# Kernel optimization log

Measured on AMD Instinct MI355X. Metric: run time of the kernel, lower is better.

Reference implementation:

```python
import jax, jax.numpy as jnp
import numpy as np

NB_T, NB_C = 4, 4
B, LT, LC, D, H = 32, 256, 128, 256, 8
E = D // H
SCALE = 1.0 / float(np.sqrt(E))


def full_attention(x, Wq, bq, Wk, bk, Wv, bv, Wo, bo):
    # x: [B, L, D]; multi-head full attention (no mask, eval-mode dropout)
    Bx, L, Dx = x.shape
    q = (x @ Wq + bq).reshape(Bx, L, H, E)
    k = (x @ Wk + bk).reshape(Bx, L, H, E)
    v = (x @ Wv + bv).reshape(Bx, L, H, E)
    scores = jnp.einsum('blhe,bshe->bhls', q, k)
    A = jax.nn.softmax(scores * SCALE, axis=-1)
    out = jnp.einsum('bhls,bshd->blhd', A, v).reshape(Bx, L, Dx)
    return out @ Wo + bo


def _branch(x, Wq, bq, Wk, bk, Wv, bv, Wo, bo, Wqi, bqi, Wki, bki, Wvi, bvi, Woi, boi):
    # x: [nb, B, L, D]; per-block intra attention (distinct weights per block)
    x_intra = jax.vmap(full_attention)(x, Wq, bq, Wk, bk, Wv, bv, Wo, bo)
    # router tokens = last token of each block -> [B, nb, D]
    routers = jnp.transpose(x_intra[:, :, -1, :], (1, 0, 2))
    x_inter = full_attention(routers, Wqi, bqi, Wki, bki, Wvi, bvi, Woi, boi)
    x_inter = jnp.transpose(x_inter, (1, 0, 2))[:, :, None, :]  # [nb, B, 1, D]
    # replace each block's router token with its inter-attended version
    return jnp.concatenate([x_intra[:, :, :-1, :], x_inter], axis=2)


def setup_inputs():
    key = jax.random.key(0)
    ks = jax.random.split(key, 32)
    s = 0.02
    inp = {}
    inp['x_t'] = jax.random.normal(ks[0], (NB_T, B, LT, D), jnp.float32)
    inp['x_c'] = jax.random.normal(ks[1], (NB_C, B, LC, D), jnp.float32)
    i = 2
    for pfx, nb in (('t', NB_T), ('c', NB_C)):
        for nm in ('q', 'k', 'v', 'o'):
            inp['W%s_%s' % (nm, pfx)] = jax.random.normal(ks[i], (nb, D, D), jnp.float32) * s
            i += 1
            inp['b%s_%s' % (nm, pfx)] = jnp.zeros((nb, D), jnp.float32)
    for pfx in ('it', 'ic'):
        for nm in ('q', 'k', 'v', 'o'):
            inp['W%s_%s' % (nm, pfx)] = jax.random.normal(ks[i], (D, D), jnp.float32) * s
            i += 1
            inp['b%s_%s' % (nm, pfx)] = jnp.zeros((D,), jnp.float32)
    return inp


def reference(x_t, x_c, Wq_t, bq_t, Wk_t, bk_t, Wv_t, bv_t, Wo_t, bo_t, Wq_c, bq_c, Wk_c, bk_c, Wv_c, bv_c, Wo_c, bo_c, Wq_it, bq_it, Wk_it, bk_it, Wv_it, bv_it, Wo_it, bo_it, Wq_ic, bq_ic, Wk_ic, bk_ic, Wv_ic, bv_ic, Wo_ic, bo_ic):
    x_out_t = _branch(x_t, Wq_t, bq_t, Wk_t, bk_t, Wv_t, bv_t, Wo_t, bo_t,
                      Wq_it, bq_it, Wk_it, bk_it, Wv_it, bv_it, Wo_it, bo_it)
    x_out_c = _branch(x_c, Wq_c, bq_c, Wk_c, bk_c, Wv_c, bv_c, Wo_c, bo_c,
                      Wq_ic, bq_ic, Wk_ic, bk_ic, Wv_ic, bv_ic, Wo_ic, bo_ic)
    return (x_out_t, x_out_c)
```

## Files before the change

kernel.cpp:

```cpp
#include <hip/hip_runtime.h>
#include <hip/hip_bf16.h>
#include <stdint.h>

#define DMODEL 256
#define HEADS 8
#define EHEAD 32
#define BATCH 32
#define NB 4
#define LT 256
#define LC 128
#define SCALE_F 0.17677669529663687f

typedef __attribute__((ext_vector_type(8))) short short8;
typedef __attribute__((ext_vector_type(4))) float f32x4;
typedef __attribute__((ext_vector_type(4))) unsigned short us4;

#define ASG __attribute__((address_space(1)))
#define ASL __attribute__((address_space(3)))

__device__ __forceinline__ unsigned short bf16_rn(float f) {
    unsigned u = __float_as_uint(f);
    u += 0x7FFFu + ((u >> 16) & 1u);
    return (unsigned short)(u >> 16);
}
__device__ __forceinline__ float bf16_f(unsigned short h) {
    return __uint_as_float(((unsigned)h) << 16);
}

__global__ void split_hi_lo(const float* __restrict__ src, unsigned short* __restrict__ hi,
                            unsigned short* __restrict__ lo, int n4)
{
    int i = blockIdx.x * blockDim.x + threadIdx.x;
    int stride = gridDim.x * blockDim.x;
    for (; i < n4; i += stride) {
        float4 a = ((const float4*)src)[i];
        float v[4] = {a.x, a.y, a.z, a.w};
        us4 h, l;
        #pragma unroll
        for (int j = 0; j < 4; ++j) {
            unsigned short hh = bf16_rn(v[j]);
            h[j] = hh;
            l[j] = bf16_rn(v[j] - bf16_f(hh));
        }
        ((us4*)hi)[i] = h;
        ((us4*)lo)[i] = l;
    }
}

__global__ __launch_bounds__(256) void transpose_split(
    const float* __restrict__ W0, const float* __restrict__ W1,
    const float* __restrict__ W2, const float* __restrict__ W3,
    unsigned short* __restrict__ H0, unsigned short* __restrict__ L0,
    unsigned short* __restrict__ H1, unsigned short* __restrict__ L1,
    unsigned short* __restrict__ H2, unsigned short* __restrict__ L2,
    unsigned short* __restrict__ H3, unsigned short* __restrict__ L3,
    int per_set)
{
    const int z   = blockIdx.z;
    const int set = z / per_set;
    const int zi  = z - set * per_set;
    const float* W; unsigned short *H, *L;
    if      (set == 0) { W = W0; H = H0; L = L0; }
    else if (set == 1) { W = W1; H = H1; L = L1; }
    else if (set == 2) { W = W2; H = H2; L = L2; }
    else               { W = W3; H = H3; L = L3; }
    W += (long long)zi * 65536;
    H += (long long)zi * 65536;
    L += (long long)zi * 65536;

    __shared__ float tile[64][65];
    const int k0 = blockIdx.y * 64, n0 = blockIdx.x * 64;
    const int c = threadIdx.x & 63, r4 = threadIdx.x >> 6;

    #pragma unroll
    for (int i = 0; i < 16; ++i) {
        int kl = r4 + i * 4;
        tile[kl][c] = W[(long long)(k0 + kl) * 256 + n0 + c];
    }
    __syncthreads();
    #pragma unroll
    for (int i = 0; i < 16; ++i) {
        int nl = r4 + i * 4;
        float v = tile[c][nl];
        unsigned short hh = bf16_rn(v);
        unsigned short ll = bf16_rn(v - bf16_f(hh));
        long long o = (long long)(n0 + nl) * 256 + k0 + c;
        H[o] = hh;
        L[o] = ll;
    }
}

template<int OUT_MODE>
__global__ __launch_bounds__(256, 2) void gemm_bf16x3_t(
    const unsigned short* __restrict__ Ah, const unsigned short* __restrict__ Al,
    const unsigned short* __restrict__ Bh, const unsigned short* __restrict__ Bl,
    const float* __restrict__ bias, void* __restrict__ Cv, float scale,
    long long sA, long long sW, long long sBias, long long sC)
{
    const int z = blockIdx.z;
    const char* aH = (const char*)(Ah + z * sA);
    const char* aL = (const char*)(Al + z * sA);
    const char* bH = (const char*)(Bh + z * sW);
    const char* bL = (const char*)(Bl + z * sW);
    const float* bz = bias + z * sBias;

    const int bm = blockIdx.y * 128;
    const int bn = blockIdx.x * 128;
    const int tid = threadIdx.x;
    const int w = tid >> 6, l = tid & 63;
    const int wr = w >> 1, wc = w & 1;
    const int lr = l & 15, lk = l >> 4;

    __shared__ __align__(16) unsigned short lds[16384];
    unsigned short* lAh = lds;
    unsigned short* lAl = lds + 4096;
    unsigned short* lBh = lds + 8192;
    unsigned short* lBl = lds + 12288;

    const int g0 = w * 64 + l;
    const int g1 = g0 + 256;
    const int row0 = g0 >> 2, kq0 = (g0 & 3) ^ ((row0 >> 1) & 3);
    const int row1 = g1 >> 2, kq1 = (g1 & 3) ^ ((row1 >> 1) & 3);
    const long long offA0 = (long long)(bm + row0) * 512 + kq0 * 16;
    const long long offA1 = (long long)(bm + row1) * 512 + kq1 * 16;
    const long long offB0 = (long long)(bn + row0) * 512 + kq0 * 16;
    const long long offB1 = (long long)(bn + row1) * 512 + kq1 * 16;

    f32x4 acc[4][4];
    #pragma unroll
    for (int m = 0; m < 4; ++m)
        #pragma unroll
        for (int n = 0; n < 4; ++n)
            acc[m][n] = (f32x4){0.f, 0.f, 0.f, 0.f};

    for (int k0 = 0; k0 < 256; k0 += 32) {
        const long long kb = (long long)k0 * 2;
        __builtin_amdgcn_global_load_lds((const ASG unsigned int*)(aH + offA0 + kb),
                                         (ASL unsigned int*)&lAh[g0 * 8], 16, 0, 0);
        __builtin_amdgcn_global_load_lds((const ASG unsigned int*)(aH + offA1 + kb),
                                         (ASL unsigned int*)&lAh[g1 * 8], 16, 0, 0);
        __builtin_amdgcn_global_load_lds((const ASG unsigned int*)(aL + offA0 + kb),
                                         (ASL unsigned int*)&lAl[g0 * 8], 16, 0, 0);
        __builtin_amdgcn_global_load_lds((const ASG unsigned int*)(aL + offA1 + kb),
                                         (ASL unsigned int*)&lAl[g1 * 8], 16, 0, 0);
        __builtin_amdgcn_global_load_lds((const ASG unsigned int*)(bH + offB0 + kb),
                                         (ASL unsigned int*)&lBh[g0 * 8], 16, 0, 0);
        __builtin_amdgcn_global_load_lds((const ASG unsigned int*)(bH + offB1 + kb),
                                         (ASL unsigned int*)&lBh[g1 * 8], 16, 0, 0);
        __builtin_amdgcn_global_load_lds((const ASG unsigned int*)(bL + offB0 + kb),
                                         (ASL unsigned int*)&lBl[g0 * 8], 16, 0, 0);
        __builtin_amdgcn_global_load_lds((const ASG unsigned int*)(bL + offB1 + kb),
                                         (ASL unsigned int*)&lBl[g1 * 8], 16, 0, 0);
        asm volatile("s_waitcnt vmcnt(0)" ::: "memory");
        __syncthreads();

        short8 fah[4], fal[4], fbh[4], fbl[4];
        #pragma unroll
        for (int m = 0; m < 4; ++m) {
            int row = wr * 64 + m * 16 + lr;
            int off = row * 32 + ((lk ^ ((row >> 1) & 3)) * 8);
            fah[m] = *(const short8*)&lAh[off];
            fal[m] = *(const short8*)&lAl[off];
        }
        #pragma unroll
        for (int n = 0; n < 4; ++n) {
            int row = wc * 64 + n * 16 + lr;
            int off = row * 32 + ((lk ^ ((row >> 1) & 3)) * 8);
            fbh[n] = *(const short8*)&lBh[off];
            fbl[n] = *(const short8*)&lBl[off];
        }
        #pragma unroll
        for (int m = 0; m < 4; ++m)
            #pragma unroll
            for (int n = 0; n < 4; ++n) {
                acc[m][n] = __builtin_amdgcn_mfma_f32_16x16x32_bf16(fah[m], fbh[n], acc[m][n], 0, 0, 0);
                acc[m][n] = __builtin_amdgcn_mfma_f32_16x16x32_bf16(fal[m], fbh[n], acc[m][n], 0, 0, 0);
                acc[m][n] = __builtin_amdgcn_mfma_f32_16x16x32_bf16(fah[m], fbl[n], acc[m][n], 0, 0, 0);
            }
        __syncthreads();
    }

    #pragma unroll
    for (int n = 0; n < 4; ++n) {
        const int col = bn + wc * 64 + n * 16 + lr;
        const float bv = bz[col];
        #pragma unroll
        for (int m = 0; m < 4; ++m) {
            const int row = bm + wr * 64 + m * 16 + lk * 4;
            #pragma unroll
            for (int j = 0; j < 4; ++j) {
                float v = acc[m][n][j] + bv;
                if (OUT_MODE == 0) {
                    ((float*)Cv)[z * sC + (long long)(row + j) * 256 + col] = v;
                } else {
                    ((unsigned short*)Cv)[z * sC + (long long)(row + j) * 256 + col] =
                        bf16_rn(v * scale);
                }
            }
        }
    }
}

template<int L>
__global__ __launch_bounds__(256) void v_transpose(
    const unsigned short* __restrict__ Vbf, unsigned short* __restrict__ VT)
{
    __shared__ unsigned short tile[L * 36];
    const int h = blockIdx.x, blkb = blockIdx.y, tid = threadIdx.x;
    const unsigned short* src = Vbf + (long long)blkb * L * 256 + h * 32;
    unsigned short* dst = VT + ((long long)blkb * HEADS + h) * 32 * L;

    #pragma unroll
    for (int i = 0; i < L * 8 / 256; ++i) {
        int ci = i * 256 + tid;
        int kv = ci >> 3, e0 = (ci & 7) * 4;
        us4 v = *(const us4*)(src + (long long)kv * 256 + e0);
        *(us4*)(&tile[kv * 36 + e0]) = v;
    }
    __syncthreads();
    #pragma unroll
    for (int i = 0; i < L * 8 / 256; ++i) {
        int ci = i * 256 + tid;
        int e = ci / (L / 4), kvc = ci % (L / 4);
        us4 v;
        #pragma unroll
        for (int j = 0; j < 4; ++j) v[j] = tile[(kvc * 4 + j) * 36 + e];
        *(us4*)(dst + (long long)e * L + kvc * 4) = v;
    }
}

template<int L>
__global__ __launch_bounds__(256) void attn_mfma(
    const unsigned short* __restrict__ Qbf, const unsigned short* __restrict__ Kbf,
    const unsigned short* __restrict__ VT,
    unsigned short* __restrict__ AOh, unsigned short* __restrict__ AOl)
{
    constexpr int KV_FRAGS    = L / 16;
    constexpr int PV_STEPS    = L / 32;
    constexpr int QT_PER_WAVE = L / 64;
    constexpr int K_BYTES     = L * 64;
    constexpr int GPR         = L / 8;

    __shared__ __align__(16) char smem[L * 256];
    unsigned short* Ks  = (unsigned short*)smem;
    unsigned short* VTs = (unsigned short*)(smem + K_BYTES);
    unsigned short* Pa  = (unsigned short*)(smem + 2 * K_BYTES);

    const int h    = blockIdx.x;
    const int blkb = blockIdx.y;
    const int tid  = threadIdx.x;
    const int w    = tid >> 6;
    const int l    = tid & 63;
    const int lq   = l & 15;
    const int lg   = l >> 4;

    const long long rowbase = (long long)blkb * L;
    const unsigned short* Kh = Kbf + rowbase * 256 + h * 32;
    const unsigned short* Qh = Qbf + rowbase * 256 + h * 32;
    const unsigned short* Vh = VT + ((long long)blkb * HEADS + h) * (32 * L);

    #pragma unroll
    for (int i = 0; i < K_BYTES / 16 / 256; ++i) {
        int gi = i * 256 + tid;
        int row = gi >> 2;
        int gsrc = (gi & 3) ^ ((row >> 1) & 3);
        __builtin_amdgcn_global_load_lds(
            (const ASG unsigned int*)(Kh + (long long)row * 256 + gsrc * 8),
            (ASL unsigned int*)(Ks + gi * 8), 16, 0, 0);
    }
    #pragma unroll
    for (int i = 0; i < K_BYTES / 16 / 256; ++i) {
        int gi = i * 256 + tid;
        int e  = gi / GPR;
        int gsrc = (gi % GPR) ^ (e & 7);
        __builtin_amdgcn_global_load_lds(
            (const ASG unsigned int*)(Vh + (long long)e * L + gsrc * 8),
            (ASL unsigned int*)(VTs + gi * 8), 16, 0, 0);
    }
    asm volatile("s_waitcnt vmcnt(0)" ::: "memory");
    __syncthreads();

    unsigned short* Pw = Pa + w * (16 * L);

    for (int qt = 0; qt < QT_PER_WAVE; ++qt) {
        const int q0 = w * (QT_PER_WAVE * 16) + qt * 16;
        short8 qf = *(const short8*)(Qh + (long long)(q0 + lq) * 256 + lg * 8);

        f32x4 sf[KV_FRAGS];
        #pragma unroll
        for (int t = 0; t < KV_FRAGS; ++t) {
            int row = t * 16 + lq;
            int off = row * 32 + ((lg ^ ((row >> 1) & 3)) * 8);
            short8 kf = *(const short8*)(Ks + off);
            sf[t] = __builtin_amdgcn_mfma_f32_16x16x32_bf16(kf, qf,
                        (f32x4){0.f, 0.f, 0.f, 0.f}, 0, 0, 0);
        }
        float lsum = 0.f;
        unsigned short pb[KV_FRAGS][4];
        #pragma unroll
        for (int t = 0; t < KV_FRAGS; ++t)
            #pragma unroll
            for (int j = 0; j < 4; ++j) {
                float s = fminf(fmaxf(sf[t][j], -60.f), 60.f);
                float p = __builtin_exp2f(s);
                lsum += p;
                pb[t][j] = bf16_rn(p);
            }
        lsum += __shfl_xor(lsum, 16);
        lsum += __shfl_xor(lsum, 32);

        #pragma unroll
        for (int t = 0; t < KV_FRAGS; ++t) {
            us4 v; v[0] = pb[t][0]; v[1] = pb[t][1]; v[2] = pb[t][2]; v[3] = pb[t][3];
            int slot = (t * 4 + lg) ^ (lq & 14);
            *(us4*)(Pw + lq * L + slot * 4) = v;
        }
        asm volatile("s_waitcnt lgkmcnt(0)" ::: "memory");

        f32x4 oacc[2] = {(f32x4){0.f,0.f,0.f,0.f}, (f32x4){0.f,0.f,0.f,0.f}};
        #pragma unroll
        for (int s = 0; s < PV_STEPS; ++s) {
            int pslot = (s * 8 + lg * 2) ^ (lq & 14);
            short8 pf = *(const short8*)(Pw + lq * L + pslot * 4);
            #pragma unroll
            for (int et = 0; et < 2; ++et) {
                int e = et * 16 + lq;
                int gk = (s * 4 + lg) ^ (e & 7);
                short8 vf = *(const short8*)(VTs + e * L + gk * 8);
                oacc[et] = __builtin_amdgcn_mfma_f32_16x16x32_bf16(pf, vf, oacc[et], 0, 0, 0);
            }
        }
        float inv[4];
        #pragma unroll
        for (int j = 0; j < 4; ++j)
            inv[j] = 1.f / __shfl(lsum, lg * 4 + j);
        #pragma unroll
        for (int et = 0; et < 2; ++et)
            #pragma unroll
            for (int j = 0; j < 4; ++j) {
                long long row = rowbase + q0 + lg * 4 + j;
                int col = h * 32 + et * 16 + lq;
                float o = oacc[et][j] * inv[j];
                unsigned short hi = bf16_rn(o);
                unsigned short lo = bf16_rn(o - bf16_f(hi));
                AOh[row * 256 + col] = hi;
                AOl[row * 256 + col] = lo;
            }
    }
}

__global__ void gather_routers(const float* __restrict__ xi, float* __restrict__ rt, int L)
{
    int t = blockIdx.x * blockDim.x + threadIdx.x;
    int d = t & 255;
    int r = t >> 8;
    int i = r & 3;
    int b = r >> 2;
    rt[(long long)r * DMODEL + d] =
        xi[(((long long)i * BATCH + b) * L + (L - 1)) * DMODEL + d];
}

__global__ void inter_attn(const float* __restrict__ RQ, const float* __restrict__ RK,
                           const float* __restrict__ RV, float* __restrict__ RA)
{
    int t = blockIdx.x * blockDim.x + threadIdx.x;
    int l = t & 3;
    int h = (t >> 2) & 7;
    int b = t >> 5;

    float q[EHEAD];
    #pragma unroll
    for (int e = 0; e < EHEAD; ++e)
        q[e] = RQ[((long long)b * 4 + l) * DMODEL + h * EHEAD + e];

    float sc[4];
    float m = -1e30f;
    #pragma unroll
    for (int s = 0; s < 4; ++s) {
        float d = 0.f;
        #pragma unroll
        for (int e = 0; e < EHEAD; ++e)
            d = fmaf(q[e], RK[((long long)b * 4 + s) * DMODEL + h * EHEAD + e], d);
        sc[s] = d * SCALE_F;
        m = fmaxf(m, sc[s]);
    }
    float lsum = 0.f;
    #pragma unroll
    for (int s = 0; s < 4; ++s) { sc[s] = __expf(sc[s] - m); lsum += sc[s]; }
    const float inv = 1.f / lsum;

    #pragma unroll
    for (int e = 0; e < EHEAD; ++e) {
        float a = 0.f;
        #pragma unroll
        for (int s = 0; s < 4; ++s)
            a = fmaf(sc[s], RV[((long long)b * 4 + s) * DMODEL + h * EHEAD + e], a);
        RA[((long long)b * 4 + l) * DMODEL + h * EHEAD + e] = a * inv;
    }
}

__global__ void scatter_routers(const float* __restrict__ ro, float* __restrict__ xi, int L)
{
    int t = blockIdx.x * blockDim.x + threadIdx.x;
    int d = t & 255;
    int r = t >> 8;
    int i = r & 3;
    int b = r >> 2;
    xi[(((long long)i * BATCH + b) * L + (L - 1)) * DMODEL + d] =
        ro[(long long)r * DMODEL + d];
}

struct BranchScratch {
    unsigned short *xh, *xl;
    unsigned short *Qbf, *Kbf, *Vbf, *VTb, *AOh, *AOl;
    unsigned short *Wth[4], *Wtl[4];
    unsigned short *WtIh[4], *WtIl[4];
    float *RT, *RQ, *RK, *RV, *RA, *RO;
    unsigned short *RTh, *RTl, *RAh, *RAl;
};

template<int L>
static void run_branch(const float* x,
    const float* Wq, const float* bq, const float* Wk, const float* bk,
    const float* Wv, const float* bv, const float* Wo, const float* bo,
    const float* Wqi, const float* bqi, const float* Wki, const float* bki,
    const float* Wvi, const float* bvi, const float* Woi, const float* boi,
    float* out, const BranchScratch& S, hipStream_t stream)
{
    const int M = BATCH * L;
    const long long sX = (long long)M * DMODEL;
    const int nTot = NB * M * DMODEL;
    const float CS = 0.17677669529663687f * 1.4426950408889634f;

    split_hi_lo<<<1024, 256, 0, stream>>>(x, S.xh, S.xl, nTot / 4);
    transpose_split<<<dim3(4, 4, 16), 256, 0, stream>>>(
        Wq, Wk, Wv, Wo,
        S.Wth[0], S.Wtl[0], S.Wth[1], S.Wtl[1],
        S.Wth[2], S.Wtl[2], S.Wth[3], S.Wtl[3], 4);

    dim3 gProj(2, M / 128, NB);
    gemm_bf16x3_t<1><<<gProj, 256, 0, stream>>>(S.xh, S.xl, S.Wth[0], S.Wtl[0], bq, S.Qbf, CS,   sX, 65536, 256, sX);
    gemm_bf16x3_t<1><<<gProj, 256, 0, stream>>>(S.xh, S.xl, S.Wth[1], S.Wtl[1], bk, S.Kbf, 1.0f, sX, 65536, 256, sX);
    gemm_bf16x3_t<1><<<gProj, 256, 0, stream>>>(S.xh, S.xl, S.Wth[2], S.Wtl[2], bv, S.Vbf, 1.0f, sX, 65536, 256, sX);

    v_transpose<L><<<dim3(HEADS, NB * BATCH), 256, 0, stream>>>(S.Vbf, S.VTb);
    attn_mfma<L><<<dim3(HEADS, NB * BATCH), 256, 0, stream>>>(S.Qbf, S.Kbf, S.VTb, S.AOh, S.AOl);

    gemm_bf16x3_t<0><<<gProj, 256, 0, stream>>>(S.AOh, S.AOl, S.Wth[3], S.Wtl[3], bo, out, 1.0f, sX, 65536, 256, sX);

    gather_routers<<<128, 256, 0, stream>>>(out, S.RT, L);
    split_hi_lo<<<32, 256, 0, stream>>>(S.RT, S.RTh, S.RTl, 128 * DMODEL / 4);
    transpose_split<<<dim3(4, 4, 4), 256, 0, stream>>>(
        Wqi, Wki, Wvi, Woi,
        S.WtIh[0], S.WtIl[0], S.WtIh[1], S.WtIl[1],
        S.WtIh[2], S.WtIl[2], S.WtIh[3], S.WtIl[3], 1);

    dim3 gI(2, 1, 1);
    gemm_bf16x3_t<0><<<gI, 256, 0, stream>>>(S.RTh, S.RTl, S.WtIh[0], S.WtIl[0], bqi, S.RQ, 1.0f, 0, 0, 0, 0);
    gemm_bf16x3_t<0><<<gI, 256, 0, stream>>>(S.RTh, S.RTl, S.WtIh[1], S.WtIl[1], bki, S.RK, 1.0f, 0, 0, 0, 0);
    gemm_bf16x3_t<0><<<gI, 256, 0, stream>>>(S.RTh, S.RTl, S.WtIh[2], S.WtIl[2], bvi, S.RV, 1.0f, 0, 0, 0, 0);

    inter_attn<<<4, 256, 0, stream>>>(S.RQ, S.RK, S.RV, S.RA);

    split_hi_lo<<<32, 256, 0, stream>>>(S.RA, S.RAh, S.RAl, 128 * DMODEL / 4);
    gemm_bf16x3_t<0><<<gI, 256, 0, stream>>>(S.RAh, S.RAl, S.WtIh[3], S.WtIl[3], boi, S.RO, 1.0f, 0, 0, 0, 0);

    scatter_routers<<<128, 256, 0, stream>>>(S.RO, out, L);
}

extern "C" void kernel_launch(void* const* d_in, const int* in_sizes, int n_in,
                              void* d_out, int out_size, void* d_ws, size_t ws_size,
                              hipStream_t stream)
{
    const float* x_t  = (const float*)d_in[0];
    const float* x_c  = (const float*)d_in[1];
    const float* Wq_t = (const float*)d_in[2];  const float* bq_t = (const float*)d_in[3];
    const float* Wk_t = (const float*)d_in[4];  const float* bk_t = (const float*)d_in[5];
    const float* Wv_t = (const float*)d_in[6];  const float* bv_t = (const float*)d_in[7];
    const float* Wo_t = (const float*)d_in[8];  const float* bo_t = (const float*)d_in[9];
    const float* Wq_c = (const float*)d_in[10]; const float* bq_c = (const float*)d_in[11];
    const float* Wk_c = (const float*)d_in[12]; const float* bk_c = (const float*)d_in[13];
    const float* Wv_c = (const float*)d_in[14]; const float* bv_c = (const float*)d_in[15];
    const float* Wo_c = (const float*)d_in[16]; const float* bo_c = (const float*)d_in[17];
    const float* Wq_it = (const float*)d_in[18]; const float* bq_it = (const float*)d_in[19];
    const float* Wk_it = (const float*)d_in[20]; const float* bk_it = (const float*)d_in[21];
    const float* Wv_it = (const float*)d_in[22]; const float* bv_it = (const float*)d_in[23];
    const float* Wo_it = (const float*)d_in[24]; const float* bo_it = (const float*)d_in[25];
    const float* Wq_ic = (const float*)d_in[26]; const float* bq_ic = (const float*)d_in[27];
    const float* Wk_ic = (const float*)d_in[28]; const float* bk_ic = (const float*)d_in[29];
    const float* Wv_ic = (const float*)d_in[30]; const float* bv_ic = (const float*)d_in[31];
    const float* Wo_ic = (const float*)d_in[32]; const float* bo_ic = (const float*)d_in[33];

    float* out = (float*)d_out;

    char* p = (char*)d_ws;
    auto alloc = [&](size_t bytes) -> char* {
        char* r = p;
        p += (bytes + 255) & ~(size_t)255;
        return r;
    };
    const size_t QKV = (size_t)NB * BATCH * LT * DMODEL;

    BranchScratch S;
    S.xh  = (unsigned short*)alloc(QKV * 2);
    S.xl  = (unsigned short*)alloc(QKV * 2);
    S.Qbf = (unsigned short*)alloc(QKV * 2);
    S.Kbf = (unsigned short*)alloc(QKV * 2);
    S.Vbf = (unsigned short*)alloc(QKV * 2);
    S.VTb = (unsigned short*)alloc(QKV * 2);
    S.AOh = (unsigned short*)alloc(QKV * 2);
    S.AOl = (unsigned short*)alloc(QKV * 2);
    for (int i = 0; i < 4; ++i) {
        S.Wth[i] = (unsigned short*)alloc((size_t)NB * 65536 * 2);
        S.Wtl[i] = (unsigned short*)alloc((size_t)NB * 65536 * 2);
    }
    for (int i = 0; i < 4; ++i) {
        S.WtIh[i] = (unsigned short*)alloc(65536 * 2);
        S.WtIl[i] = (unsigned short*)alloc(65536 * 2);
    }
    S.RT = (float*)alloc(128 * DMODEL * 4);
    S.RQ = (float*)alloc(128 * DMODEL * 4);
    S.RK = (float*)alloc(128 * DMODEL * 4);
    S.RV = (float*)alloc(128 * DMODEL * 4);
    S.RA = (float*)alloc(128 * DMODEL * 4);
    S.RO = (float*)alloc(128 * DMODEL * 4);
    S.RTh = (unsigned short*)alloc(128 * DMODEL * 2);
    S.RTl = (unsigned short*)alloc(128 * DMODEL * 2);
    S.RAh = (unsigned short*)alloc(128 * DMODEL * 2);
    S.RAl = (unsigned short*)alloc(128 * DMODEL * 2);

    run_branch<LT>(x_t, Wq_t, bq_t, Wk_t, bk_t, Wv_t, bv_t, Wo_t, bo_t,
                   Wq_it, bq_it, Wk_it, bk_it, Wv_it, bv_it, Wo_it, bo_it,
                   out, S, stream);

    float* out_c = out + (size_t)NB * BATCH * LT * DMODEL;
    run_branch<LC>(x_c, Wq_c, bq_c, Wk_c, bk_c, Wv_c, bv_c, Wo_c, bo_c,
                   Wq_ic, bq_ic, Wk_ic, bk_ic, Wv_ic, bv_ic, Wo_ic, bo_ic,
                   out_c, S, stream);
}
```

Measured before the change: 516.0 us.

## Fuse QKV projections with V-transpose epilogue and merge small prep/split kernels

Combines the three Q/K/V projection GEMMs into one launch whose V epilogue writes the head-transposed layout directly, removing the separate V buffer and transpose kernel. Weight prep for intra and inter weights is merged into a single launch, and hi/lo bf16 splitting is folded into the router gather and inter-attention kernels. The inter-attention QKV GEMMs are batched into one launch, and the attention kernel's P staging is reorganized per step. Scattered 2-byte stores for V^T and a higher occupancy target may cost bandwidth or registers.

```diff
diff --git a/kernel.cpp b/kernel.cpp
--- a/kernel.cpp
+++ b/kernel.cpp
@@ -9,7 +9,6 @@
 #define NB 4
 #define LT 256
 #define LC 128
-#define SCALE_F 0.17677669529663687f
 
 typedef __attribute__((ext_vector_type(8))) short short8;
 typedef __attribute__((ext_vector_type(4))) float f32x4;
@@ -47,26 +46,20 @@
     }
 }
 
-__global__ __launch_bounds__(256) void transpose_split(
-    const float* __restrict__ W0, const float* __restrict__ W1,
-    const float* __restrict__ W2, const float* __restrict__ W3,
-    unsigned short* __restrict__ H0, unsigned short* __restrict__ L0,
-    unsigned short* __restrict__ H1, unsigned short* __restrict__ L1,
-    unsigned short* __restrict__ H2, unsigned short* __restrict__ L2,
-    unsigned short* __restrict__ H3, unsigned short* __restrict__ L3,
-    int per_set)
-{
-    const int z   = blockIdx.z;
-    const int set = z / per_set;
-    const int zi  = z - set * per_set;
-    const float* W; unsigned short *H, *L;
-    if      (set == 0) { W = W0; H = H0; L = L0; }
-    else if (set == 1) { W = W1; H = H1; L = L1; }
-    else if (set == 2) { W = W2; H = H2; L = L2; }
-    else               { W = W3; H = H3; L = L3; }
-    W += (long long)zi * 65536;
-    H += (long long)zi * 65536;
-    L += (long long)zi * 65536;
+struct PrepArgs {
+    const float* W[8];
+    unsigned short* H[8];
+    unsigned short* Lo[8];
+};
+
+__global__ __launch_bounds__(256) void prep_weights(PrepArgs pa)
+{
+    const int z = blockIdx.z;
+    int set, zi;
+    if (z < 16) { set = z >> 2; zi = z & 3; } else { set = 4 + (z - 16); zi = 0; }
+    const float* W = pa.W[set] + (long long)zi * 65536;
+    unsigned short* H = pa.H[set] + (long long)zi * 65536;
+    unsigned short* L = pa.Lo[set] + (long long)zi * 65536;
 
     __shared__ float tile[64][65];
     const int k0 = blockIdx.y * 64, n0 = blockIdx.x * 64;
@@ -90,158 +83,180 @@
     }
 }
 
-template<int OUT_MODE>
-__global__ __launch_bounds__(256, 2) void gemm_bf16x3_t(
+#define GEMM_BODY(aH, aL, bH, bL)                                                   \
+    const int bm = blockIdx.y * 128;                                                \
+    const int bn = blockIdx.x * 128;                                                \
+    const int tid = threadIdx.x;                                                    \
+    const int w = tid >> 6, l = tid & 63;                                           \
+    const int wr = w >> 1, wc = w & 1;                                              \
+    const int lr = l & 15, lk = l >> 4;                                             \
+    __shared__ __align__(16) unsigned short lds[16384];                             \
+    unsigned short* lAh = lds;                                                      \
+    unsigned short* lAl = lds + 4096;                                               \
+    unsigned short* lBh = lds + 8192;                                               \
+    unsigned short* lBl = lds + 12288;                                              \
+    const int g0 = w * 64 + l;                                                      \
+    const int g1 = g0 + 256;                                                        \
+    const int row0 = g0 >> 2, kq0 = (g0 & 3) ^ ((row0 >> 1) & 3);                   \
+    const int row1 = g1 >> 2, kq1 = (g1 & 3) ^ ((row1 >> 1) & 3);                   \
+    const long long offA0 = (long long)(bm + row0) * 512 + kq0 * 16;                \
+    const long long offA1 = (long long)(bm + row1) * 512 + kq1 * 16;                \
+    const long long offB0 = (long long)(bn + row0) * 512 + kq0 * 16;                \
+    const long long offB1 = (long long)(bn + row1) * 512 + kq1 * 16;                \
+    f32x4 acc[4][4];                                                                \
+    _Pragma("unroll")                                                               \
+    for (int m = 0; m < 4; ++m)                                                     \
+        _Pragma("unroll")                                                           \
+        for (int n = 0; n < 4; ++n)                                                 \
+            acc[m][n] = (f32x4){0.f, 0.f, 0.f, 0.f};                                \
+    for (int k0 = 0; k0 < 256; k0 += 32) {                                          \
+        const long long kb = (long long)k0 * 2;                                     \
+        __builtin_amdgcn_global_load_lds((const ASG unsigned int*)(aH + offA0 + kb),\
+                                         (ASL unsigned int*)&lAh[g0 * 8], 16, 0, 0);\
+        __builtin_amdgcn_global_load_lds((const ASG unsigned int*)(aH + offA1 + kb),\
+                                         (ASL unsigned int*)&lAh[g1 * 8], 16, 0, 0);\
+        __builtin_amdgcn_global_load_lds((const ASG unsigned int*)(aL + offA0 + kb),\
+                                         (ASL unsigned int*)&lAl[g0 * 8], 16, 0, 0);\
+        __builtin_amdgcn_global_load_lds((const ASG unsigned int*)(aL + offA1 + kb),\
+                                         (ASL unsigned int*)&lAl[g1 * 8], 16, 0, 0);\
+        __builtin_amdgcn_global_load_lds((const ASG unsigned int*)(bH + offB0 + kb),\
+                                         (ASL unsigned int*)&lBh[g0 * 8], 16, 0, 0);\
+        __builtin_amdgcn_global_load_lds((const ASG unsigned int*)(bH + offB1 + kb),\
+                                         (ASL unsigned int*)&lBh[g1 * 8], 16, 0, 0);\
+        __builtin_amdgcn_global_load_lds((const ASG unsigned int*)(bL + offB0 + kb),\
+                                         (ASL unsigned int*)&lBl[g0 * 8], 16, 0, 0);\
+        __builtin_amdgcn_global_load_lds((const ASG unsigned int*)(bL + offB1 + kb),\
+                                         (ASL unsigned int*)&lBl[g1 * 8], 16, 0, 0);\
+        asm volatile("s_waitcnt vmcnt(0)" ::: "memory");                            \
+        __syncthreads();                                                            \
+        short8 fah[4], fal[4], fbh[4], fbl[4];                                      \
+        _Pragma("unroll")                                                           \
+        for (int m = 0; m < 4; ++m) {                                               \
+            int row = wr * 64 + m * 16 + lr;                                        \
+            int off = row * 32 + ((lk ^ ((row >> 1) & 3)) * 8);                     \
+            fah[m] = *(const short8*)&lAh[off];                                     \
+            fal[m] = *(const short8*)&lAl[off];                                     \
+        }                                                                           \
+        _Pragma("unroll")                                                           \
+        for (int n = 0; n < 4; ++n) {                                               \
+            int row = wc * 64 + n * 16 + lr;                                        \
+            int off = row * 32 + ((lk ^ ((row >> 1) & 3)) * 8);                     \
+            fbh[n] = *(const short8*)&lBh[off];                                     \
+            fbl[n] = *(const short8*)&lBl[off];                                     \
+        }                                                                           \
+        _Pragma("unroll")                                                           \
+        for (int m = 0; m < 4; ++m)                                                 \
+            _Pragma("unroll")                                                       \
+            for (int n = 0; n < 4; ++n) {                                           \
+                acc[m][n] = __builtin_amdgcn_mfma_f32_16x16x32_bf16(fah[m], fbh[n], acc[m][n], 0, 0, 0); \
+                acc[m][n] = __builtin_amdgcn_mfma_f32_16x16x32_bf16(fal[m], fbh[n], acc[m][n], 0, 0, 0); \
+                acc[m][n] = __builtin_amdgcn_mfma_f32_16x16x32_bf16(fah[m], fbl[n], acc[m][n], 0, 0, 0); \
+            }                                                                       \
+        __syncthreads();                                                            \
+    }
+
+__global__ __launch_bounds__(256, 3) void gemm_qkv(
     const unsigned short* __restrict__ Ah, const unsigned short* __restrict__ Al,
-    const unsigned short* __restrict__ Bh, const unsigned short* __restrict__ Bl,
-    const float* __restrict__ bias, void* __restrict__ Cv, float scale,
-    long long sA, long long sW, long long sBias, long long sC)
+    const unsigned short* __restrict__ Wbase,
+    const float* __restrict__ bq, const float* __restrict__ bk, const float* __restrict__ bv,
+    unsigned short* __restrict__ Qout, unsigned short* __restrict__ Kout,
+    unsigned short* __restrict__ VTout,
+    float qscale, int M, int kvShift)
+{
+    const int zAll = blockIdx.z;
+    const int proj = zAll >> 2;
+    const int zb   = zAll & 3;
+    const long long sX = (long long)M * 256;
+    const char* aH = (const char*)(Ah + zb * sX);
+    const char* aL = (const char*)(Al + zb * sX);
+    const long long wOff = (long long)proj * (2LL * NB * 65536) + (long long)zb * 65536;
+    const char* bH = (const char*)(Wbase + wOff);
+    const char* bL = (const char*)(Wbase + wOff + NB * 65536);
+    const float* bz = (proj == 0 ? bq : proj == 1 ? bk : bv) + zb * 256;
+
+    GEMM_BODY(aH, aL, bH, bL)
+
+    if (proj < 2) {
+        unsigned short* C = (proj == 0 ? Qout : Kout) + zb * sX;
+        const float sc = (proj == 0) ? qscale : 1.0f;
+        #pragma unroll
+        for (int n = 0; n < 4; ++n) {
+            const int col = bn + wc * 64 + n * 16 + lr;
+            const float bv_ = bz[col];
+            #pragma unroll
+            for (int m = 0; m < 4; ++m) {
+                const int row = bm + wr * 64 + m * 16 + lk * 4;
+                #pragma unroll
+                for (int j = 0; j < 4; ++j)
+                    C[(long long)(row + j) * 256 + col] = bf16_rn((acc[m][n][j] + bv_) * sc);
+            }
+        }
+    } else {
+        const int Lkv = 1 << kvShift;
+        #pragma unroll
+        for (int n = 0; n < 4; ++n) {
+            const int col = bn + wc * 64 + n * 16 + lr;
+            const int hh = col >> 5, e = col & 31;
+            const float bv_ = bz[col];
+            #pragma unroll
+            for (int m = 0; m < 4; ++m) {
+                const int row = bm + wr * 64 + m * 16 + lk * 4;
+                #pragma unroll
+                for (int j = 0; j < 4; ++j) {
+                    const int r = row + j;
+                    const int blkb = zb * BATCH + (r >> kvShift);
+                    const long long dst =
+                        ((((long long)blkb * HEADS + hh) * 32 + e) << kvShift) + (r & (Lkv - 1));
+                    VTout[dst] = bf16_rn(acc[m][n][j] + bv_);
+                }
+            }
+        }
+    }
+}
+
+struct Bias4 { const float* p[4]; };
+
+__global__ __launch_bounds__(256, 3) void gemm_f32out(
+    const unsigned short* __restrict__ Ah, const unsigned short* __restrict__ Al,
+    const unsigned short* __restrict__ Bh_, const unsigned short* __restrict__ Bl_,
+    Bias4 b4, float* __restrict__ C,
+    long long sA, long long sW, long long sC)
 {
     const int z = blockIdx.z;
     const char* aH = (const char*)(Ah + z * sA);
     const char* aL = (const char*)(Al + z * sA);
-    const char* bH = (const char*)(Bh + z * sW);
-    const char* bL = (const char*)(Bl + z * sW);
-    const float* bz = bias + z * sBias;
-
-    const int bm = blockIdx.y * 128;
-    const int bn = blockIdx.x * 128;
-    const int tid = threadIdx.x;
-    const int w = tid >> 6, l = tid & 63;
-    const int wr = w >> 1, wc = w & 1;
-    const int lr = l & 15, lk = l >> 4;
-
-    __shared__ __align__(16) unsigned short lds[16384];
-    unsigned short* lAh = lds;
-    unsigned short* lAl = lds + 4096;
-    unsigned short* lBh = lds + 8192;
-    unsigned short* lBl = lds + 12288;
-
-    const int g0 = w * 64 + l;
-    const int g1 = g0 + 256;
-    const int row0 = g0 >> 2, kq0 = (g0 & 3) ^ ((row0 >> 1) & 3);
-    const int row1 = g1 >> 2, kq1 = (g1 & 3) ^ ((row1 >> 1) & 3);
-    const long long offA0 = (long long)(bm + row0) * 512 + kq0 * 16;
-    const long long offA1 = (long long)(bm + row1) * 512 + kq1 * 16;
-    const long long offB0 = (long long)(bn + row0) * 512 + kq0 * 16;
-    const long long offB1 = (long long)(bn + row1) * 512 + kq1 * 16;
-
-    f32x4 acc[4][4];
-    #pragma unroll
-    for (int m = 0; m < 4; ++m)
-        #pragma unroll
-        for (int n = 0; n < 4; ++n)
-            acc[m][n] = (f32x4){0.f, 0.f, 0.f, 0.f};
-
-    for (int k0 = 0; k0 < 256; k0 += 32) {
-        const long long kb = (long long)k0 * 2;
-        __builtin_amdgcn_global_load_lds((const ASG unsigned int*)(aH + offA0 + kb),
-                                         (ASL unsigned int*)&lAh[g0 * 8], 16, 0, 0);
-        __builtin_amdgcn_global_load_lds((const ASG unsigned int*)(aH + offA1 + kb),
-                                         (ASL unsigned int*)&lAh[g1 * 8], 16, 0, 0);
-        __builtin_amdgcn_global_load_lds((const ASG unsigned int*)(aL + offA0 + kb),
-                                         (ASL unsigned int*)&lAl[g0 * 8], 16, 0, 0);
-        __builtin_amdgcn_global_load_lds((const ASG unsigned int*)(aL + offA1 + kb),
-                                         (ASL unsigned int*)&lAl[g1 * 8], 16, 0, 0);
-        __builtin_amdgcn_global_load_lds((const ASG unsigned int*)(bH + offB0 + kb),
-                                         (ASL unsigned int*)&lBh[g0 * 8], 16, 0, 0);
-        __builtin_amdgcn_global_load_lds((const ASG unsigned int*)(bH + offB1 + kb),
-                                         (ASL unsigned int*)&lBh[g1 * 8], 16, 0, 0);
-        __builtin_amdgcn_global_load_lds((const ASG unsigned int*)(bL + offB0 + kb),
-                                         (ASL unsigned int*)&lBl[g0 * 8], 16, 0, 0);
-        __builtin_amdgcn_global_load_lds((const ASG unsigned int*)(bL + offB1 + kb),
-                                         (ASL unsigned int*)&lBl[g1 * 8], 16, 0, 0);
-        asm volatile("s_waitcnt vmcnt(0)" ::: "memory");
-        __syncthreads();
-
-        short8 fah[4], fal[4], fbh[4], fbl[4];
-        #pragma unroll
-        for (int m = 0; m < 4; ++m) {
-            int row = wr * 64 + m * 16 + lr;
-            int off = row * 32 + ((lk ^ ((row >> 1) & 3)) * 8);
-            fah[m] = *(const short8*)&lAh[off];
-            fal[m] = *(const short8*)&lAl[off];
-        }
-        #pragma unroll
-        for (int n = 0; n < 4; ++n) {
-            int row = wc * 64 + n * 16 + lr;
-            int off = row * 32 + ((lk ^ ((row >> 1) & 3)) * 8);
-            fbh[n] = *(const short8*)&lBh[off];
-            fbl[n] = *(const short8*)&lBl[off];
-        }
-        #pragma unroll
-        for (int m = 0; m < 4; ++m)
-            #pragma unroll
-            for (int n = 0; n < 4; ++n) {
-                acc[m][n] = __builtin_amdgcn_mfma_f32_16x16x32_bf16(fah[m], fbh[n], acc[m][n], 0, 0, 0);
-                acc[m][n] = __builtin_amdgcn_mfma_f32_16x16x32_bf16(fal[m], fbh[n], acc[m][n], 0, 0, 0);
-                acc[m][n] = __builtin_amdgcn_mfma_f32_16x16x32_bf16(fah[m], fbl[n], acc[m][n], 0, 0, 0);
-            }
-        __syncthreads();
-    }
+    const char* bH = (const char*)(Bh_ + z * sW);
+    const char* bL = (const char*)(Bl_ + z * sW);
+    const float* bz = b4.p[z];
+
+    GEMM_BODY(aH, aL, bH, bL)
 
     #pragma unroll
     for (int n = 0; n < 4; ++n) {
         const int col = bn + wc * 64 + n * 16 + lr;
-        const float bv = bz[col];
+        const float bv_ = bz[col];
         #pragma unroll
         for (int m = 0; m < 4; ++m) {
             const int row = bm + wr * 64 + m * 16 + lk * 4;
             #pragma unroll
-            for (int j = 0; j < 4; ++j) {
-                float v = acc[m][n][j] + bv;
-                if (OUT_MODE == 0) {
-                    ((float*)Cv)[z * sC + (long long)(row + j) * 256 + col] = v;
-                } else {
-                    ((unsigned short*)Cv)[z * sC + (long long)(row + j) * 256 + col] =
-                        bf16_rn(v * scale);
-                }
-            }
+            for (int j = 0; j < 4; ++j)
+                C[z * sC + (long long)(row + j) * 256 + col] = acc[m][n][j] + bv_;
         }
     }
 }
 
 template<int L>
-__global__ __launch_bounds__(256) void v_transpose(
-    const unsigned short* __restrict__ Vbf, unsigned short* __restrict__ VT)
-{
-    __shared__ unsigned short tile[L * 36];
-    const int h = blockIdx.x, blkb = blockIdx.y, tid = threadIdx.x;
-    const unsigned short* src = Vbf + (long long)blkb * L * 256 + h * 32;
-    unsigned short* dst = VT + ((long long)blkb * HEADS + h) * 32 * L;
-
-    #pragma unroll
-    for (int i = 0; i < L * 8 / 256; ++i) {
-        int ci = i * 256 + tid;
-        int kv = ci >> 3, e0 = (ci & 7) * 4;
-        us4 v = *(const us4*)(src + (long long)kv * 256 + e0);
-        *(us4*)(&tile[kv * 36 + e0]) = v;
-    }
-    __syncthreads();
-    #pragma unroll
-    for (int i = 0; i < L * 8 / 256; ++i) {
-        int ci = i * 256 + tid;
-        int e = ci / (L / 4), kvc = ci % (L / 4);
-        us4 v;
-        #pragma unroll
-        for (int j = 0; j < 4; ++j) v[j] = tile[(kvc * 4 + j) * 36 + e];
-        *(us4*)(dst + (long long)e * L + kvc * 4) = v;
-    }
-}
-
-template<int L>
-__global__ __launch_bounds__(256) void attn_mfma(
+__global__ __launch_bounds__(256, 4) void attn_mfma(
     const unsigned short* __restrict__ Qbf, const unsigned short* __restrict__ Kbf,
     const unsigned short* __restrict__ VT,
     unsigned short* __restrict__ AOh, unsigned short* __restrict__ AOl)
 {
-    constexpr int KV_FRAGS    = L / 16;
-    constexpr int PV_STEPS    = L / 32;
     constexpr int QT_PER_WAVE = L / 64;
-    constexpr int K_BYTES     = L * 64;
-    constexpr int GPR         = L / 8;
-
-    __shared__ __align__(16) char smem[L * 256];
+    constexpr int NS      = L / 32;
+    constexpr int K_BYTES = L * 64;
+    constexpr int GPR     = L / 8;
+
+    __shared__ __align__(16) char smem[2 * K_BYTES + 4 * 2048];
     unsigned short* Ks  = (unsigned short*)smem;
     unsigned short* VTs = (unsigned short*)(smem + K_BYTES);
     unsigned short* Pa  = (unsigned short*)(smem + 2 * K_BYTES);
@@ -253,11 +268,19 @@
     const int l    = tid & 63;
     const int lq   = l & 15;
     const int lg   = l >> 4;
+    const int a3   = (lq >> 2) & 3;
 
     const long long rowbase = (long long)blkb * L;
     const unsigned short* Kh = Kbf + rowbase * 256 + h * 32;
     const unsigned short* Qh = Qbf + rowbase * 256 + h * 32;
     const unsigned short* Vh = VT + ((long long)blkb * HEADS + h) * (32 * L);
+
+    short8 qf[QT_PER_WAVE];
+    #pragma unroll
+    for (int qt = 0; qt < QT_PER_WAVE; ++qt) {
+        int q0 = w * (QT_PER_WAVE * 16) + qt * 16;
+        qf[qt] = *(const short8*)(Qh + (long long)(q0 + lq) * 256 + lg * 8);
+    }
 
     #pragma unroll
     for (int i = 0; i < K_BYTES / 16 / 256; ++i) {
@@ -280,48 +303,39 @@
     asm volatile("s_waitcnt vmcnt(0)" ::: "memory");
     __syncthreads();
 
-    unsigned short* Pw = Pa + w * (16 * L);
-
+    unsigned short* Pw = Pa + w * 1024;
+
+    #pragma unroll
     for (int qt = 0; qt < QT_PER_WAVE; ++qt) {
         const int q0 = w * (QT_PER_WAVE * 16) + qt * 16;
-        short8 qf = *(const short8*)(Qh + (long long)(q0 + lq) * 256 + lg * 8);
-
-        f32x4 sf[KV_FRAGS];
-        #pragma unroll
-        for (int t = 0; t < KV_FRAGS; ++t) {
-            int row = t * 16 + lq;
-            int off = row * 32 + ((lg ^ ((row >> 1) & 3)) * 8);
-            short8 kf = *(const short8*)(Ks + off);
-            sf[t] = __builtin_amdgcn_mfma_f32_16x16x32_bf16(kf, qf,
-                        (f32x4){0.f, 0.f, 0.f, 0.f}, 0, 0, 0);
-        }
+        f32x4 oacc[2] = {(f32x4){0.f,0.f,0.f,0.f}, (f32x4){0.f,0.f,0.f,0.f}};
         float lsum = 0.f;
-        unsigned short pb[KV_FRAGS][4];
-        #pragma unroll
-        for (int t = 0; t < KV_FRAGS; ++t)
+
+        #pragma unroll
+        for (int s = 0; s < NS; ++s) {
+            unsigned short* Ps = Pw + (s & 1) * 512;
             #pragma unroll
-            for (int j = 0; j < 4; ++j) {
-                float s = fminf(fmaxf(sf[t][j], -60.f), 60.f);
-                float p = __builtin_exp2f(s);
-                lsum += p;
-                pb[t][j] = bf16_rn(p);
+            for (int t2 = 0; t2 < 2; ++t2) {
+                int row = s * 32 + t2 * 16 + lq;
+                int off = row * 32 + ((lg ^ ((row >> 1) & 3)) * 8);
+                short8 kf = *(const short8*)(Ks + off);
+                f32x4 sf = __builtin_amdgcn_mfma_f32_16x16x32_bf16(
+                               kf, qf[qt], (f32x4){0.f,0.f,0.f,0.f}, 0, 0, 0);
+                float p0 = __builtin_exp2f(fminf(sf[0], 60.f));
+                float p1 = __builtin_exp2f(fminf(sf[1], 60.f));
+                float p2 = __builtin_exp2f(fminf(sf[2], 60.f));
+                float p3 = __builtin_exp2f(fminf(sf[3], 60.f));
+                lsum += (p0 + p1) + (p2 + p3);
+                unsigned r0, r1;
+                asm("v_cvt_pk_bf16_f32 %0, %1, %2" : "=v"(r0) : "v"(p0), "v"(p1));
+                asm("v_cvt_pk_bf16_f32 %0, %1, %2" : "=v"(r1) : "v"(p2), "v"(p3));
+                int phys = (t2 * 4 + lg) ^ (a3 << 1);
+                uint2 wv; wv.x = r0; wv.y = r1;
+                *(uint2*)(Ps + lq * 32 + phys * 4) = wv;
             }
-        lsum += __shfl_xor(lsum, 16);
-        lsum += __shfl_xor(lsum, 32);
-
-        #pragma unroll
-        for (int t = 0; t < KV_FRAGS; ++t) {
-            us4 v; v[0] = pb[t][0]; v[1] = pb[t][1]; v[2] = pb[t][2]; v[3] = pb[t][3];
-            int slot = (t * 4 + lg) ^ (lq & 14);
-            *(us4*)(Pw + lq * L + slot * 4) = v;
-        }
-        asm volatile("s_waitcnt lgkmcnt(0)" ::: "memory");
-
-        f32x4 oacc[2] = {(f32x4){0.f,0.f,0.f,0.f}, (f32x4){0.f,0.f,0.f,0.f}};
-        #pragma unroll
-        for (int s = 0; s < PV_STEPS; ++s) {
-            int pslot = (s * 8 + lg * 2) ^ (lq & 14);
-            short8 pf = *(const short8*)(Pw + lq * L + pslot * 4);
+            asm volatile("s_waitcnt lgkmcnt(0)" ::: "memory");
+            int pair = (lg ^ a3) << 1;
+            short8 pf = *(const short8*)(Ps + lq * 32 + pair * 4);
             #pragma unroll
             for (int et = 0; et < 2; ++et) {
                 int e = et * 16 + lq;
@@ -330,10 +344,14 @@
                 oacc[et] = __builtin_amdgcn_mfma_f32_16x16x32_bf16(pf, vf, oacc[et], 0, 0, 0);
             }
         }
+
+        lsum += __shfl_xor(lsum, 16);
+        lsum += __shfl_xor(lsum, 32);
         float inv[4];
         #pragma unroll
         for (int j = 0; j < 4; ++j)
             inv[j] = 1.f / __shfl(lsum, lg * 4 + j);
+
         #pragma unroll
         for (int et = 0; et < 2; ++et)
             #pragma unroll
@@ -349,20 +367,26 @@
     }
 }
 
-__global__ void gather_routers(const float* __restrict__ xi, float* __restrict__ rt, int L)
+__global__ void gather_split(const float* __restrict__ xi,
+                             unsigned short* __restrict__ RTh,
+                             unsigned short* __restrict__ RTl, int L)
 {
     int t = blockIdx.x * blockDim.x + threadIdx.x;
     int d = t & 255;
     int r = t >> 8;
     int i = r & 3;
     int b = r >> 2;
-    rt[(long long)r * DMODEL + d] =
-        xi[(((long long)i * BATCH + b) * L + (L - 1)) * DMODEL + d];
+    float v = xi[(((long long)i * BATCH + b) * L + (L - 1)) * DMODEL + d];
+    unsigned short hh = bf16_rn(v);
+    RTh[(long long)r * DMODEL + d] = hh;
+    RTl[(long long)r * DMODEL + d] = bf16_rn(v - bf16_f(hh));
 }
 
 __global__ void inter_attn(const float* __restrict__ RQ, const float* __restrict__ RK,
-                           const float* __restrict__ RV, float* __restrict__ RA)
-{
+                           const float* __restrict__ RV,
+                           unsigned short* __restrict__ RAh, unsigned short* __restrict__ RAl)
+{
+    const float SCALE_F = 0.17677669529663687f;
     int t = blockIdx.x * blockDim.x + threadIdx.x;
     int l = t & 3;
     int h = (t >> 2) & 7;
@@ -395,7 +419,10 @@
         #pragma unroll
         for (int s = 0; s < 4; ++s)
             a = fmaf(sc[s], RV[((long long)b * 4 + s) * DMODEL + h * EHEAD + e], a);
-        RA[((long long)b * 4 + l) * DMODEL + h * EHEAD + e] = a * inv;
+        float o = a * inv;
+        unsigned short hh = bf16_rn(o);
+        RAh[((long long)b * 4 + l) * DMODEL + h * EHEAD + e] = hh;
+        RAl[((long long)b * 4 + l) * DMODEL + h * EHEAD + e] = bf16_rn(o - bf16_f(hh));
     }
 }
 
@@ -412,11 +439,11 @@
 
 struct BranchScratch {
     unsigned short *xh, *xl;
-    unsigned short *Qbf, *Kbf, *Vbf, *VTb, *AOh, *AOl;
+    unsigned short *Qbf, *Kbf, *VTb, *AOh, *AOl;
     unsigned short *Wth[4], *Wtl[4];
     unsigned short *WtIh[4], *WtIl[4];
-    float *RT, *RQ, *RK, *RV, *RA, *RO;
     unsigned short *RTh, *RTl, *RAh, *RAl;
+    float *RQKV, *RO;
 };
 
 template<int L>
@@ -430,40 +457,40 @@
     const int M = BATCH * L;
     const long long sX = (long long)M * DMODEL;
     const int nTot = NB * M * DMODEL;
+    const int kvShift = (L == 256) ? 8 : 7;
     const float CS = 0.17677669529663687f * 1.4426950408889634f;
 
     split_hi_lo<<<1024, 256, 0, stream>>>(x, S.xh, S.xl, nTot / 4);
-    transpose_split<<<dim3(4, 4, 16), 256, 0, stream>>>(
-        Wq, Wk, Wv, Wo,
-        S.Wth[0], S.Wtl[0], S.Wth[1], S.Wtl[1],
-        S.Wth[2], S.Wtl[2], S.Wth[3], S.Wtl[3], 4);
-
-    dim3 gProj(2, M / 128, NB);
-    gemm_bf16x3_t<1><<<gProj, 256, 0, stream>>>(S.xh, S.xl, S.Wth[0], S.Wtl[0], bq, S.Qbf, CS,   sX, 65536, 256, sX);
-    gemm_bf16x3_t<1><<<gProj, 256, 0, stream>>>(S.xh, S.xl, S.Wth[1], S.Wtl[1], bk, S.Kbf, 1.0f, sX, 65536, 256, sX);
-    gemm_bf16x3_t<1><<<gProj, 256, 0, stream>>>(S.xh, S.xl, S.Wth[2], S.Wtl[2], bv, S.Vbf, 1.0f, sX, 65536, 256, sX);
-
-    v_transpose<L><<<dim3(HEADS, NB * BATCH), 256, 0, stream>>>(S.Vbf, S.VTb);
-    attn_mfma<L><<<dim3(HEADS, NB * BATCH), 256, 0, stream>>>(S.Qbf, S.Kbf, S.VTb, S.AOh, S.AOl);
-
-    gemm_bf16x3_t<0><<<gProj, 256, 0, stream>>>(S.AOh, S.AOl, S.Wth[3], S.Wtl[3], bo, out, 1.0f, sX, 65536, 256, sX);
-
-    gather_routers<<<128, 256, 0, stream>>>(out, S.RT, L);
-    split_hi_lo<<<32, 256, 0, stream>>>(S.RT, S.RTh, S.RTl, 128 * DMODEL / 4);
-    transpose_split<<<dim3(4, 4, 4), 256, 0, stream>>>(
-        Wqi, Wki, Wvi, Woi,
-        S.WtIh[0], S.WtIl[0], S.WtIh[1], S.WtIl[1],
-        S.WtIh[2], S.WtIl[2], S.WtIh[3], S.WtIl[3], 1);
-
-    dim3 gI(2, 1, 1);
-    gemm_bf16x3_t<0><<<gI, 256, 0, stream>>>(S.RTh, S.RTl, S.WtIh[0], S.WtIl[0], bqi, S.RQ, 1.0f, 0, 0, 0, 0);
-    gemm_bf16x3_t<0><<<gI, 256, 0, stream>>>(S.RTh, S.RTl, S.WtIh[1], S.WtIl[1], bki, S.RK, 1.0f, 0, 0, 0, 0);
-    gemm_bf16x3_t<0><<<gI, 256, 0, stream>>>(S.RTh, S.RTl, S.WtIh[2], S.WtIl[2], bvi, S.RV, 1.0f, 0, 0, 0, 0);
-
-    inter_attn<<<4, 256, 0, stream>>>(S.RQ, S.RK, S.RV, S.RA);
-
-    split_hi_lo<<<32, 256, 0, stream>>>(S.RA, S.RAh, S.RAl, 128 * DMODEL / 4);
-    gemm_bf16x3_t<0><<<gI, 256, 0, stream>>>(S.RAh, S.RAl, S.WtIh[3], S.WtIl[3], boi, S.RO, 1.0f, 0, 0, 0, 0);
+
+    PrepArgs pa;
+    pa.W[0] = Wq;  pa.W[1] = Wk;  pa.W[2] = Wv;  pa.W[3] = Wo;
+    pa.W[4] = Wqi; pa.W[5] = Wki; pa.W[6] = Wvi; pa.W[7] = Woi;
+    for (int i = 0; i < 4; ++i) { pa.H[i] = S.Wth[i];  pa.Lo[i] = S.Wtl[i]; }
+    for (int i = 0; i < 4; ++i) { pa.H[4+i] = S.WtIh[i]; pa.Lo[4+i] = S.WtIl[i]; }
+    prep_weights<<<dim3(4, 4, 20), 256, 0, stream>>>(pa);
+
+    gemm_qkv<<<dim3(2, M / 128, 12), 256, 0, stream>>>(
+        S.xh, S.xl, S.Wth[0], bq, bk, bv, S.Qbf, S.Kbf, S.VTb, CS, M, kvShift);
+
+    attn_mfma<L><<<dim3(HEADS, NB * BATCH), 256, 0, stream>>>(
+        S.Qbf, S.Kbf, S.VTb, S.AOh, S.AOl);
+
+    Bias4 b4o = {{bo, bo + 256, bo + 512, bo + 768}};
+    gemm_f32out<<<dim3(2, M / 128, NB), 256, 0, stream>>>(
+        S.AOh, S.AOl, S.Wth[3], S.Wtl[3], b4o, out, sX, 65536, sX);
+
+    gather_split<<<128, 256, 0, stream>>>(out, S.RTh, S.RTl, L);
+
+    Bias4 b4i = {{bqi, bki, bvi, nullptr}};
+    gemm_f32out<<<dim3(2, 1, 3), 256, 0, stream>>>(
+        S.RTh, S.RTl, S.WtIh[0], S.WtIl[0], b4i, S.RQKV, 0, 131072, 32768);
+
+    inter_attn<<<4, 256, 0, stream>>>(S.RQKV, S.RQKV + 32768, S.RQKV + 65536,
+                                      S.RAh, S.RAl);
+
+    Bias4 b4r = {{boi, nullptr, nullptr, nullptr}};
+    gemm_f32out<<<dim3(2, 1, 1), 256, 0, stream>>>(
+        S.RAh, S.RAl, S.WtIh[3], S.WtIl[3], b4r, S.RO, 0, 0, 0);
 
     scatter_routers<<<128, 256, 0, stream>>>(S.RO, out, L);
 }
@@ -506,7 +533,6 @@
     S.xl  = (unsigned short*)alloc(QKV * 2);
     S.Qbf = (unsigned short*)alloc(QKV * 2);
     S.Kbf = (unsigned short*)alloc(QKV * 2);
-    S.Vbf = (unsigned short*)alloc(QKV * 2);
     S.VTb = (unsigned short*)alloc(QKV * 2);
     S.AOh = (unsigned short*)alloc(QKV * 2);
     S.AOl = (unsigned short*)alloc(QKV * 2);
@@ -518,16 +544,12 @@
         S.WtIh[i] = (unsigned short*)alloc(65536 * 2);
         S.WtIl[i] = (unsigned short*)alloc(65536 * 2);
     }
-    S.RT = (float*)alloc(128 * DMODEL * 4);
-    S.RQ = (float*)alloc(128 * DMODEL * 4);
-    S.RK = (float*)alloc(128 * DMODEL * 4);
-    S.RV = (float*)alloc(128 * DMODEL * 4);
-    S.RA = (float*)alloc(128 * DMODEL * 4);
-    S.RO = (float*)alloc(128 * DMODEL * 4);
-    S.RTh = (unsigned short*)alloc(128 * DMODEL * 2);
-    S.RTl = (unsigned short*)alloc(128 * DMODEL * 2);
-    S.RAh = (unsigned short*)alloc(128 * DMODEL * 2);
-    S.RAl = (unsigned short*)alloc(128 * DMODEL * 2);
+    S.RTh  = (unsigned short*)alloc(128 * DMODEL * 2);
+    S.RTl  = (unsigned short*)alloc(128 * DMODEL * 2);
+    S.RAh  = (unsigned short*)alloc(128 * DMODEL * 2);
+    S.RAl  = (unsigned short*)alloc(128 * DMODEL * 2);
+    S.RQKV = (float*)alloc(3 * 128 * DMODEL * 4);
+    S.RO   = (float*)alloc(128 * DMODEL * 4);
 
     run_branch<LT>(x_t, Wq_t, bq_t, Wk_t, bk_t, Wv_t, bv_t, Wo_t, bo_t,
                    Wq_it, bq_it, Wk_it, bk_it, Wv_it, bv_it, Wo_it, bo_it,
```

Result: faster. 431.1 us (-16.5%).
